# Kernel optimization log

Hardware: AMD Instinct MI355X
Metric: run time of the kernel (lower is better)

The kernel has to match this reference:

```python
import jax, jax.numpy as jnp
import numpy as np

DECAY = 0.99
EPS = 1e-05


def setup_inputs() -> dict:
    key = jax.random.key(0)
    k1, k2 = jax.random.split(key)
    B, L, D, K = 8, 2048, 512, 4096
    x = jax.random.normal(k1, (B, L, D), dtype=jnp.float32)
    # variance_scaling(scale=1, fan_in, uniform): U(-limit, limit), limit = sqrt(3/fan_in)
    limit = np.sqrt(3.0 / D)
    codebook = jax.random.uniform(k2, (K, D), dtype=jnp.float32, minval=-limit, maxval=limit)
    return {
        "x": x,
        "codebook": codebook,
        "hidden_cluster": jnp.zeros((K,), jnp.float32),
        "hidden_dw": jnp.zeros((K, D), jnp.float32),
        "count": jnp.zeros((), jnp.float32),
    }


def reference(x, codebook, hidden_cluster, hidden_dw, count):
    K, D = codebook.shape
    B, L, _ = x.shape
    # avoids materializing the (B,L,K,D) broadcast the naive cdist creates)
    x2 = jnp.sum(x * x, axis=-1, keepdims=True)                  # (B,L,1)
    c2 = jnp.sum(codebook * codebook, axis=-1)                   # (K,)
    xc = jnp.einsum("bld,kd->blk", x, codebook)                  # (B,L,K)
    d2 = x2 - 2.0 * xc + c2
    indices = jnp.argmin(d2, axis=-1)                            # (B,L) int
    flat_idx = indices.reshape(-1)

    # cluster_counts = one_hot(indices).sum((0,1)) as a scatter-add
    cluster_counts = jnp.zeros((K,), jnp.float32).at[flat_idx].add(1.0)
    # dw = einsum('bln,bld->nd', one_hot, x) as a scatter-add of x rows
    dw = jnp.zeros((K, D), jnp.float32).at[flat_idx].add(x.reshape(-1, D))

    decay = jnp.asarray(DECAY, x.dtype)
    one = jnp.ones([], x.dtype)
    count_new = count + 1.0
    bias = one - decay ** count_new

    hidden_cluster_new = hidden_cluster * decay + (one - decay) * cluster_counts
    avg_cluster = hidden_cluster_new / bias
    hidden_dw_new = hidden_dw * decay + (one - decay) * dw
    avg_dw = hidden_dw_new / bias

    N = jnp.sum(avg_cluster)
    cc = (avg_cluster + EPS) / (N + K * EPS) * N
    codebook_new = avg_dw / cc[:, None]

    # quantized = one_hot(indices) @ codebook_new == gather
    q = codebook_new[indices]                                    # (B,L,D)
    quantized = x + jax.lax.stop_gradient(q - x)
    # optax.l2_loss(x, quantized).mean() == 0.5*(x-quantized)^2 mean
    codebook_loss = 0.5 * jnp.mean(jnp.square(x - quantized))
    return quantized, codebook_loss, indices
```

## Files before the change

kernel.cpp:

```cpp
#include <hip/hip_runtime.h>
#include <math.h>

#define BL 16384
#define D  512
#define K  4096
#define NCHB 8
#define XLOFF 8388608

#define OFF_C2    0
#define OFF_X2    (16<<10)
#define OFF_CNT   (80<<10)
#define OFF_AVGC  (96<<10)
#define OFF_SCAL  (112<<10)
#define OFF_IDX16 (116<<10)
#define OFF_KEYS  (160<<10)
#define OFF_CAND  (288<<10)
#define OFF_CBP   (576<<10)
#define OFF_CBN_FB (256<<10)

typedef _Float16 f16x8 __attribute__((ext_vector_type(8)));
typedef float    f32x4 __attribute__((ext_vector_type(4)));
#define MFMA16(a,b,c) __builtin_amdgcn_mfma_f32_16x16x32_f16(a,b,c,0,0,0)


__global__ void rowsq_all(const float* __restrict__ x, const float* __restrict__ cb,
                          float* __restrict__ x2, float* __restrict__ c2)
{
    int b    = blockIdx.x;
    int lane = threadIdx.x;
    const float* p; float* o; int row;
    if (b < K) { p = cb; o = c2; row = b; }
    else       { p = x;  o = x2; row = b - K; }
    p += (size_t)row * D;
    float s = 0.f;
#pragma unroll
    for (int j = 0; j < D / 64; ++j) {
        float v = p[lane + j * 64];
        s = fmaf(v, v, s);
    }
#pragma unroll
    for (int off = 32; off > 0; off >>= 1)
        s += __shfl_down(s, off, 64);
    if (lane == 0) o[row] = s;
}

__global__ __launch_bounds__(256) void rescore_kernel(
    const float* __restrict__ x, const float* __restrict__ cb,
    const float* __restrict__ x2, const float* __restrict__ c2,
    const unsigned short* __restrict__ cand,
    unsigned long long* __restrict__ keys,
    float* __restrict__ counts, unsigned short* __restrict__ idx16)
{
    int t = blockIdx.x * 256 + threadIdx.x;
    int row = t >> 3, ci = t & 7;
    int idx = cand[(size_t)row * 8 + ci];
    const float* xp = x  + (size_t)row * D;
    const float* cp = cb + (size_t)idx * D;
    float acc = 0.f;
#pragma unroll 4
    for (int k0 = 0; k0 < D; k0 += 4) {
        float4 xv = *(const float4*)(xp + k0);
        float4 cv = *(const float4*)(cp + k0);
        acc = fmaf(xv.x, cv.x, acc);
        acc = fmaf(xv.y, cv.y, acc);
        acc = fmaf(xv.z, cv.z, acc);
        acc = fmaf(xv.w, cv.w, acc);
    }
    float wv = x2[row] - 2.0f * acc;
    float dd = wv + c2[idx];
    unsigned long long key =
        ((unsigned long long)__float_as_uint(dd) << 12) | (unsigned long long)idx;
#pragma unroll
    for (int m = 1; m < 8; m <<= 1) {
        unsigned long long o = __shfl_xor(key, m, 64);
        key = o < key ? o : key;
    }
    if ((t & 7) == 0) {
        keys[row] = key;
        int kf = (int)(key & 0xFFFULL);
        idx16[row] = (unsigned short)kf;
        atomicAdd(&counts[kf], 1.0f);
    }
}


__device__ __forceinline__ void load_lds16(const unsigned short* g, unsigned short* l) {
    __builtin_amdgcn_global_load_lds(
        (const __attribute__((address_space(1))) unsigned int*)(g),
        (__attribute__((address_space(3))) unsigned int*)(l), 16, 0, 0);
}

__global__ __launch_bounds__(256) void split_interleave(
    const float* __restrict__ x, const float* __restrict__ cb,
    unsigned short* __restrict__ xp, unsigned short* __restrict__ cbp)
{
    int gw   = blockIdx.x * 4 + (threadIdx.x >> 6);
    int lane = threadIdx.x & 63;
    int rl   = lane >> 3;
    int p    = lane & 7;
    const float* src; int nr, c, r0; bool isX;
    if (gw < 16384) { c = gw >> 11; r0 = (gw & 2047) * 8; src = x;  nr = BL; isX = true; }
    else { int lw = gw - 16384; c = lw >> 9; r0 = (lw & 511) * 8; src = cb; nr = K; isX = false; }
    int r = r0 + rl;
    int g = p ^ rl;
    const float* sp = src + (size_t)r * D + c * 64 + g * 8;
    float4 f0 = *(const float4*)sp, f1 = *(const float4*)(sp + 4);
    float f[8] = {f0.x,f0.y,f0.z,f0.w,f1.x,f1.y,f1.z,f1.w};
    __align__(16) _Float16 oh[8], ol[8];
#pragma unroll
    for (int i = 0; i < 8; ++i) {
        _Float16 h = (_Float16)f[i];
        oh[i] = h;
        ol[i] = (_Float16)(f[i] - (float)h);
    }
    size_t off = ((size_t)(c * nr + r) * 8 + p) * 8;
    if (isX) {
        *(uint4*)(xp + off)         = *(const uint4*)oh;
        *(uint4*)(xp + XLOFF + off) = *(const uint4*)ol;
    } else {
        *(uint4*)(cbp + off) = *(const uint4*)oh;
    }
}

__global__ __launch_bounds__(512, 2) void argmin_mfma(
    const unsigned short* __restrict__ xp, const unsigned short* __restrict__ cbp,
    const float* __restrict__ x2, const float* __restrict__ c2,
    unsigned short* __restrict__ cand)
{
    __shared__ __align__(16) unsigned short buf[2 * 32768];
    __shared__ __align__(16) float c2s[1024];
    __shared__ __align__(16) float x2s[128];

#define AH_OFF 0
#define AL_OFF 16384
#define B_OFF  32768

    const int tid = threadIdx.x;
    const int l   = tid & 63;
    const int q   = l >> 4;
    const int cc  = l & 15;
    const int w   = tid >> 6;
    const int wm  = w >> 2;
    const int wn  = w & 3;
    const int row0 = blockIdx.x * 128;
    const int nb   = blockIdx.y * 1024;

    char* sb = (char*)buf;

    int rdA[4], rdB[4];
#pragma unroll
    for (int t = 0; t < 4; ++t) {
        int ra = wm * 64 + t * 16 + cc;
        int rb = wn * 64 + t * 16 + cc;
        rdA[t] = ra * 128 + ((q ^ (ra & 7)) * 16);
        rdB[t] = rb * 128 + ((q ^ (rb & 7)) * 16);
    }

    if (tid < 128) x2s[tid] = x2[row0 + tid];
#pragma unroll
    for (int j = 0; j < 2; ++j) c2s[tid + j * 512] = c2[nb + tid + j * 512];
    {
        const unsigned short* sAh0 = xp + ((size_t)row0 << 6);
        const unsigned short* sAl0 = sAh0 + XLOFF;
        const unsigned short* sB0  = cbp + ((size_t)nb << 6);
#pragma unroll
        for (int i = 0; i < 2; ++i) {
            load_lds16(sAh0 + i * 4096 + tid * 8,
                       (unsigned short*)(sb + AH_OFF + i * 8192 + tid * 16));
            load_lds16(sAl0 + i * 4096 + tid * 8,
                       (unsigned short*)(sb + AL_OFF + i * 8192 + tid * 16));
        }
#pragma unroll
        for (int i = 0; i < 4; ++i)
            load_lds16(sB0 + i * 4096 + tid * 8,
                       (unsigned short*)(sb + B_OFF + i * 8192 + tid * 16));
    }
    asm volatile("s_waitcnt vmcnt(0) lgkmcnt(0)" ::: "memory");
    __builtin_amdgcn_s_barrier();

    unsigned long long k1[16], k2[16];
#pragma unroll
    for (int s = 0; s < 16; ++s) { k1[s] = ~0ULL; k2[s] = ~0ULL; }

    f32x4 acc[4][4];
#pragma unroll
    for (int tm = 0; tm < 4; ++tm)
#pragma unroll
        for (int tn = 0; tn < 4; ++tn) { f32x4 z = {0.f,0.f,0.f,0.f}; acc[tm][tn] = z; }

#pragma unroll 1
    for (int it = 0; it < 32; ++it) {
        const bool pf = (it < 31);
        const int  br = (it & 1) << 16;
        const int  bw = br ^ 65536;
        const int  it1 = it + 1;
        const int  c1  = it1 & 7;
        const int  n01 = (it1 >> 3) & 3;
        const unsigned short* srcAh = xp + ((size_t)(c1 * BL + row0) << 6);
        const unsigned short* srcAl = srcAh + XLOFF;
        const unsigned short* srcB  = cbp + ((size_t)(c1 * K + nb + n01 * 256) << 6);

        f16x8 Ah[4], Bf[4];
#pragma unroll
        for (int t = 0; t < 4; ++t) {
            Ah[t] = *(const f16x8*)(sb + br + AH_OFF + rdA[t]);
            Bf[t] = *(const f16x8*)(sb + br + B_OFF  + rdB[t]);
        }
        if (pf) {
#pragma unroll
            for (int i = 0; i < 2; ++i)
                load_lds16(srcAh + i * 4096 + tid * 8,
                           (unsigned short*)(sb + bw + AH_OFF + i * 8192 + tid * 16));
            asm volatile("s_waitcnt vmcnt(2)" ::: "memory");
        } else {
            asm volatile("s_waitcnt vmcnt(0)" ::: "memory");
        }
        __builtin_amdgcn_s_barrier();
        asm volatile("s_waitcnt lgkmcnt(0)" ::: "memory");
        __builtin_amdgcn_sched_barrier(0);
        __builtin_amdgcn_s_setprio(1);
#pragma unroll
        for (int tm = 0; tm < 4; ++tm)
#pragma unroll
            for (int tn = 0; tn < 4; ++tn)
                acc[tm][tn] = MFMA16(Ah[tm], Bf[tn], acc[tm][tn]);
        __builtin_amdgcn_s_setprio(0);
        __builtin_amdgcn_s_barrier();

        f16x8 Al[4];
#pragma unroll
        for (int t = 0; t < 4; ++t)
            Al[t] = *(const f16x8*)(sb + br + AL_OFF + rdA[t]);
        if (pf) {
#pragma unroll
            for (int i = 0; i < 2; ++i)
                load_lds16(srcB + i * 4096 + tid * 8,
                           (unsigned short*)(sb + bw + B_OFF + i * 8192 + tid * 16));
        }
        __builtin_amdgcn_s_barrier();
        asm volatile("s_waitcnt lgkmcnt(0)" ::: "memory");
        __builtin_amdgcn_sched_barrier(0);
        __builtin_amdgcn_s_setprio(1);
#pragma unroll
        for (int tm = 0; tm < 4; ++tm)
#pragma unroll
            for (int tn = 0; tn < 4; ++tn)
                acc[tm][tn] = MFMA16(Al[tm], Bf[tn], acc[tm][tn]);
        __builtin_amdgcn_s_setprio(0);
        __builtin_amdgcn_s_barrier();

        f16x8 Ah1[4], Bg[4];
#pragma unroll
        for (int t = 0; t < 4; ++t) {
            Ah1[t] = *(const f16x8*)(sb + br + AH_OFF + (rdA[t] ^ 64));
            Bg[t]  = *(const f16x8*)(sb + br + B_OFF  + (rdB[t] ^ 64));
        }
        if (pf) {
#pragma unroll
            for (int i = 2; i < 4; ++i)
                load_lds16(srcB + i * 4096 + tid * 8,
                           (unsigned short*)(sb + bw + B_OFF + i * 8192 + tid * 16));
        }
        __builtin_amdgcn_s_barrier();
        asm volatile("s_waitcnt lgkmcnt(0)" ::: "memory");
        __builtin_amdgcn_sched_barrier(0);
        __builtin_amdgcn_s_setprio(1);
#pragma unroll
        for (int tm = 0; tm < 4; ++tm)
#pragma unroll
            for (int tn = 0; tn < 4; ++tn)
                acc[tm][tn] = MFMA16(Ah1[tm], Bg[tn], acc[tm][tn]);
        __builtin_amdgcn_s_setprio(0);
        __builtin_amdgcn_s_barrier();

        f16x8 Al1[4];
#pragma unroll
        for (int t = 0; t < 4; ++t)
            Al1[t] = *(const f16x8*)(sb + br + AL_OFF + (rdA[t] ^ 64));
        if (pf) {
#pragma unroll
            for (int i = 0; i < 2; ++i)
                load_lds16(srcAl + i * 4096 + tid * 8,
                           (unsigned short*)(sb + bw + AL_OFF + i * 8192 + tid * 16));
            asm volatile("s_waitcnt vmcnt(2)" ::: "memory");
        }
        __builtin_amdgcn_s_barrier();
        asm volatile("s_waitcnt lgkmcnt(0)" ::: "memory");
        __builtin_amdgcn_sched_barrier(0);
        __builtin_amdgcn_s_setprio(1);
#pragma unroll
        for (int tm = 0; tm < 4; ++tm)
#pragma unroll
            for (int tn = 0; tn < 4; ++tn)
                acc[tm][tn] = MFMA16(Al1[tm], Bg[tn], acc[tm][tn]);
        __builtin_amdgcn_s_setprio(0);
        __builtin_amdgcn_s_barrier();

        if ((it & 7) == 7) {
            const int n0 = it >> 3;
            float c2v[4];
#pragma unroll
            for (int tn = 0; tn < 4; ++tn)
                c2v[tn] = c2s[n0 * 256 + wn * 64 + tn * 16 + cc];
#pragma unroll
            for (int tm = 0; tm < 4; ++tm)
#pragma unroll
                for (int r = 0; r < 4; ++r) {
                    const int s = tm * 4 + r;
                    float x2v = x2s[wm * 64 + tm * 16 + q * 4 + r];
#pragma unroll
                    for (int tn = 0; tn < 4; ++tn) {
                        unsigned col = nb + n0 * 256 + wn * 64 + tn * 16 + cc;
                        float dd = (x2v - 2.0f * acc[tm][tn][r]) + c2v[tn];
                        unsigned long long key =
                            ((unsigned long long)__float_as_uint(dd) << 12) | col;
                        if (key < k1[s]) { k2[s] = k1[s]; k1[s] = key; }
                        else if (key < k2[s]) { k2[s] = key; }
                    }
                }
#pragma unroll
            for (int tm = 0; tm < 4; ++tm)
#pragma unroll
                for (int tn = 0; tn < 4; ++tn) { f32x4 z = {0.f,0.f,0.f,0.f}; acc[tm][tn] = z; }
        }
    }

#pragma unroll
    for (int s = 0; s < 16; ++s) {
#pragma unroll
        for (int m = 1; m < 16; m <<= 1) {
            unsigned long long o1 = __shfl_xor(k1[s], m, 64);
            unsigned long long o2 = __shfl_xor(k2[s], m, 64);
            unsigned long long lf = k1[s] > o1 ? k1[s] : o1;
            unsigned long long ws_ = k2[s] < o2 ? k2[s] : o2;
            k1[s] = k1[s] < o1 ? k1[s] : o1;
            k2[s] = lf < ws_ ? lf : ws_;
        }
    }

    __syncthreads();
    unsigned long long* sc = (unsigned long long*)buf;
    if (cc == 0) {
#pragma unroll
        for (int s = 0; s < 16; ++s) {
            int rl = wm * 64 + (s >> 2) * 16 + q * 4 + (s & 3);
            sc[(rl * 4 + wn) * 2 + 0] = k1[s];
            sc[(rl * 4 + wn) * 2 + 1] = k2[s];
        }
    }
    __syncthreads();
    if (tid < 128) {
        unsigned long long m1 = sc[(tid * 4 + 0) * 2 + 0];
        unsigned long long m2 = sc[(tid * 4 + 0) * 2 + 1];
#pragma unroll
        for (int j = 1; j < 4; ++j) {
            unsigned long long b1 = sc[(tid * 4 + j) * 2 + 0];
            unsigned long long b2 = sc[(tid * 4 + j) * 2 + 1];
            unsigned long long lf = m1 > b1 ? m1 : b1;
            unsigned long long ws_ = m2 < b2 ? m2 : b2;
            m1 = m1 < b1 ? m1 : b1;
            m2 = lf < ws_ ? lf : ws_;
        }
        size_t base = (size_t)(row0 + tid) * 8 + blockIdx.y * 2;
        cand[base + 0] = (unsigned short)(m1 & 0xFFFULL);
        cand[base + 1] = (unsigned short)(m2 & 0xFFFULL);
    }
}

__global__ __launch_bounds__(256) void argmin_fb(
    const float* __restrict__ x, const float* __restrict__ cb,
    const float* __restrict__ x2, const float* __restrict__ c2,
    unsigned long long* __restrict__ keys)
{
    __shared__ __align__(16) float As[32][68];
    __shared__ __align__(16) float Bs[32][68];
    __shared__ float rv[64][16];
    __shared__ int   ri[64][16];

    const int tid  = threadIdx.x;
    const int tx   = tid & 15;
    const int ty   = tid >> 4;
    const int row0 = blockIdx.x * 64;
    const int nb   = blockIdx.y * 1024;

    float x2r[4];
#pragma unroll
    for (int m = 0; m < 4; ++m) x2r[m] = x2[row0 + ty * 4 + m];

    float minv[4]; int mini[4];
#pragma unroll
    for (int m = 0; m < 4; ++m) { minv[m] = 3.4028235e38f; mini[m] = 0; }

    for (int n0 = 0; n0 < 1024; n0 += 64) {
        float acc[4][4];
#pragma unroll
        for (int m = 0; m < 4; ++m)
#pragma unroll
            for (int n = 0; n < 4; ++n) acc[m][n] = 0.f;

        for (int d0 = 0; d0 < D; d0 += 32) {
            __syncthreads();
#pragma unroll
            for (int j = 0; j < 2; ++j) {
                int v   = j * 256 + tid;
                int row = v >> 3;
                int col = (v & 7) * 4;
                float4 av = *(const float4*)(x  + (size_t)(row0 + row) * D + d0 + col);
                As[col + 0][row] = av.x; As[col + 1][row] = av.y;
                As[col + 2][row] = av.z; As[col + 3][row] = av.w;
                float4 bv = *(const float4*)(cb + (size_t)(nb + n0 + row) * D + d0 + col);
                Bs[col + 0][row] = bv.x; Bs[col + 1][row] = bv.y;
                Bs[col + 2][row] = bv.z; Bs[col + 3][row] = bv.w;
            }
            __syncthreads();
#pragma unroll
            for (int kk = 0; kk < 32; ++kk) {
                float4 a4 = *(const float4*)&As[kk][ty * 4];
                float4 b4 = *(const float4*)&Bs[kk][tx * 4];
                float a_[4] = { a4.x, a4.y, a4.z, a4.w };
                float b_[4] = { b4.x, b4.y, b4.z, b4.w };
#pragma unroll
                for (int m = 0; m < 4; ++m)
#pragma unroll
                    for (int n = 0; n < 4; ++n)
                        acc[m][n] = fmaf(a_[m], b_[n], acc[m][n]);
            }
        }
#pragma unroll
        for (int n = 0; n < 4; ++n) {
            int kidx = nb + n0 + tx * 4 + n;
            float c2k = c2[kidx];
#pragma unroll
            for (int m = 0; m < 4; ++m) {
                float wv = x2r[m] - 2.0f * acc[m][n];
                float dd = wv + c2k;
                if (dd < minv[m]) { minv[m] = dd; mini[m] = kidx; }
            }
        }
    }
#pragma unroll
    for (int m = 0; m < 4; ++m) { rv[ty * 4 + m][tx] = minv[m]; ri[ty * 4 + m][tx] = mini[m]; }
    __syncthreads();
    if (tid < 64) {
        float bv = rv[tid][0]; int bi = ri[tid][0];
#pragma unroll
        for (int j = 1; j < 16; ++j) {
            float v = rv[tid][j]; int ii = ri[tid][j];
            if (v < bv || (v == bv && ii < bi)) { bv = v; bi = ii; }
        }
        unsigned long long key =
            ((unsigned long long)__float_as_uint(bv) << 12) | (unsigned long long)bi;
        atomicMin(&keys[row0 + tid], key);
    }
}


__global__ void count_kernel(const unsigned long long* __restrict__ keys,
                             float* __restrict__ counts, unsigned short* __restrict__ idx16)
{
    int i = blockIdx.x * 256 + threadIdx.x;
    int k = (int)(keys[i] & 0xFFFULL);
    idx16[i] = (unsigned short)k;
    atomicAdd(&counts[k], 1.0f);
}

__global__ __launch_bounds__(256) void ema_cluster_kernel(
    const float* __restrict__ hc, const float* __restrict__ counts,
    const float* __restrict__ countp, float* __restrict__ avgc, float* __restrict__ Nout)
{
    __shared__ float sm[256];
    int i = blockIdx.x * 256 + threadIdx.x;
    const float om = 1.0f - 0.99f;
    float bias = 1.0f - powf(0.99f, countp[0] + 1.0f);
    float a = (hc[i] * 0.99f + om * counts[i]) / bias;
    avgc[i] = a;
    sm[threadIdx.x] = a;
    __syncthreads();
    for (int s = 128; s > 0; s >>= 1) {
        if (threadIdx.x < s) sm[threadIdx.x] += sm[threadIdx.x + s];
        __syncthreads();
    }
    if (threadIdx.x == 0) atomicAdd(Nout, sm[0]);
}

__global__ __launch_bounds__(256) void code_update_kernel(
    const float* __restrict__ x, const unsigned short* __restrict__ idx16,
    const float* __restrict__ hdw, const float* __restrict__ avgc,
    const float* __restrict__ Nptr, const float* __restrict__ countp,
    float* __restrict__ cbn)
{
    __shared__ unsigned short rows[2048];
    __shared__ int cnt;
    int k = blockIdx.x, tid = threadIdx.x;
    if (tid == 0) cnt = 0;
    __syncthreads();
    const uint4* ip = (const uint4*)idx16;
    for (int j = 0; j < 8; ++j) {
        int u = j * 256 + tid;
        uint4 v = ip[u];
        unsigned ww[4] = {v.x, v.y, v.z, v.w};
#pragma unroll
        for (int e = 0; e < 4; ++e) {
            int k0 = (int)(ww[e] & 0xFFFFu), k1 = (int)(ww[e] >> 16);
            if (k0 == k) { int p = atomicAdd(&cnt, 1); if (p < 2048) rows[p] = (unsigned short)(u * 8 + e * 2); }
            if (k1 == k) { int p = atomicAdd(&cnt, 1); if (p < 2048) rows[p] = (unsigned short)(u * 8 + e * 2 + 1); }
        }
    }
    __syncthreads();
    int n = cnt < 2048 ? cnt : 2048;
    float a0 = 0.f, a1 = 0.f;
    for (int p = 0; p < n; ++p) {
        int r = rows[p];
        a0 += x[(size_t)r * D + tid];
        a1 += x[(size_t)r * D + tid + 256];
    }
    const float om = 1.0f - 0.99f;
    float bias = 1.0f - powf(0.99f, countp[0] + 1.0f);
    float Nv = *Nptr;
    float ccv = ((avgc[k] + 1e-5f) / (Nv + 0.04096f)) * Nv;
    size_t b = (size_t)k * D;
    cbn[b + tid]       = ((hdw[b + tid]       * 0.99f + om * a0) / bias) / ccv;
    cbn[b + tid + 256] = ((hdw[b + tid + 256] * 0.99f + om * a1) / bias) / ccv;
}

__global__ __launch_bounds__(256) void gather_kernel(
    const float* __restrict__ x, const unsigned long long* __restrict__ keys,
    const float* __restrict__ cbn, float* __restrict__ outq,
    float* __restrict__ partial)
{
    __shared__ float sm[256];
    int row = blockIdx.x;
    int tid = threadIdx.x;
    int k   = (int)(keys[row] & 0xFFFULL);
    const float* xpp = x   + (size_t)row * D;
    const float* cp  = cbn + (size_t)k   * D;
    float* op = outq + (size_t)row * D;
    float local = 0.f;
#pragma unroll
    for (int j = 0; j < 2; ++j) {
        int d = tid + j * 256;
        float xv = xpp[d];
        float qv = cp[d];
        float quant = xv + (qv - xv);
        op[d] = quant;
        float diff = xv - quant;
        local = fmaf(diff, diff, local);
    }
    sm[tid] = local;
    __syncthreads();
    for (int s = 128; s > 0; s >>= 1) {
        if (tid < s) sm[tid] += sm[tid + s];
        __syncthreads();
    }
    if (tid == 0) {
        partial[row] = sm[0];
        outq[8388609 + row] = (float)k;
    }
}

__global__ __launch_bounds__(256) void finalize_kernel(
    const float* __restrict__ partial, float* __restrict__ out)
{
    __shared__ double sm[256];
    int tid = threadIdx.x;
    double s = 0.0;
#pragma unroll
    for (int j = 0; j < 64; ++j) s += (double)partial[tid + j * 256];
    sm[tid] = s;
    __syncthreads();
    for (int st = 128; st > 0; st >>= 1) {
        if (tid < st) sm[tid] += sm[tid + st];
        __syncthreads();
    }
    if (tid == 0) out[8388608] = (float)(0.5 * sm[0] / 8388608.0);
}


extern "C" void kernel_launch(void* const* d_in, const int* in_sizes, int n_in,
                              void* d_out, int out_size, void* d_ws, size_t ws_size,
                              hipStream_t stream)
{
    const float* x   = (const float*)d_in[0];
    const float* cb  = (const float*)d_in[1];
    const float* hc  = (const float*)d_in[2];
    const float* hdw = (const float*)d_in[3];
    const float* cnt = (const float*)d_in[4];
    float* out = (float*)d_out;

    char* ws = (char*)d_ws;
    float*  c2     = (float*)(ws + OFF_C2);
    float*  x2     = (float*)(ws + OFF_X2);
    float*  counts = (float*)(ws + OFF_CNT);
    float*  avgc   = (float*)(ws + OFF_AVGC);
    float*  Nout   = (float*)(ws + OFF_SCAL + 8);
    unsigned short* idx16 = (unsigned short*)(ws + OFF_IDX16);
    unsigned long long* keys = (unsigned long long*)(ws + OFF_KEYS);
    float*  partial= (float*)(ws + OFF_X2);

    hipMemsetAsync(ws + OFF_CNT, 0, (32 << 10) + 16, stream);

    rowsq_all<<<K + BL, 64, 0, stream>>>(x, cb, x2, c2);

    const bool primary = ws_size >= ((size_t)10 << 20);
    float* cbn;
    if (primary) {
        unsigned short* gxp = (unsigned short*)d_out;
        unsigned short* gcp = (unsigned short*)(ws + OFF_CBP);
        unsigned short* cand = (unsigned short*)(ws + OFF_CAND);
        cbn = (float*)(ws + OFF_CBP);

        split_interleave<<<5120, 256, 0, stream>>>(x, cb, gxp, gcp);
        argmin_mfma<<<dim3(BL / 128, 4), 512, 0, stream>>>(gxp, gcp, x2, c2, cand);
        rescore_kernel<<<(BL * 8) / 256, 256, 0, stream>>>(x, cb, x2, c2, cand, keys,
                                                           counts, idx16);
    } else {
        cbn = (float*)(ws + OFF_CBN_FB);
        hipMemsetAsync(ws + OFF_KEYS, 0xFF, BL * 8, stream);
        argmin_fb<<<dim3(BL / 64, 4), 256, 0, stream>>>(x, cb, x2, c2, keys);
        count_kernel<<<BL / 256, 256, 0, stream>>>(keys, counts, idx16);
    }

    ema_cluster_kernel<<<K / 256, 256, 0, stream>>>(hc, counts, cnt, avgc, Nout);
    code_update_kernel<<<K, 256, 0, stream>>>(x, idx16, hdw, avgc, Nout, cnt, cbn);
    gather_kernel<<<BL, 256, 0, stream>>>(x, keys, cbn, out, partial);
    finalize_kernel<<<1, 256, 0, stream>>>(partial, out);
}
```

Before: 349.5 us.

## Issue all next-stage LDS prefetches upfront and use one barrier per iteration

```diff
diff --git a/kernel.cpp b/kernel.cpp
--- a/kernel.cpp
+++ b/kernel.cpp
@@ -193,12 +193,28 @@
         const bool pf = (it < 31);
         const int  br = (it & 1) << 16;
         const int  bw = br ^ 65536;
-        const int  it1 = it + 1;
-        const int  c1  = it1 & 7;
-        const int  n01 = (it1 >> 3) & 3;
-        const unsigned short* srcAh = xp + ((size_t)(c1 * BL + row0) << 6);
-        const unsigned short* srcAl = srcAh + XLOFF;
-        const unsigned short* srcB  = cbp + ((size_t)(c1 * K + nb + n01 * 256) << 6);
+
+        if (pf) {
+            const int it1 = it + 1;
+            const int c1  = it1 & 7;
+            const int n01 = (it1 >> 3) & 3;
+            const unsigned short* srcAh = xp + ((size_t)(c1 * BL + row0) << 6);
+            const unsigned short* srcAl = srcAh + XLOFF;
+            const unsigned short* srcB  = cbp + ((size_t)(c1 * K + nb + n01 * 256) << 6);
+#pragma unroll
+            for (int i = 0; i < 2; ++i)
+                load_lds16(srcAh + i * 4096 + tid * 8,
+                           (unsigned short*)(sb + bw + AH_OFF + i * 8192 + tid * 16));
+#pragma unroll
+            for (int i = 0; i < 2; ++i)
+                load_lds16(srcAl + i * 4096 + tid * 8,
+                           (unsigned short*)(sb + bw + AL_OFF + i * 8192 + tid * 16));
+#pragma unroll
+            for (int i = 0; i < 4; ++i)
+                load_lds16(srcB + i * 4096 + tid * 8,
+                           (unsigned short*)(sb + bw + B_OFF + i * 8192 + tid * 16));
+            __builtin_amdgcn_sched_barrier(0);
+        }
 
         f16x8 Ah[4], Bf[4];
 #pragma unroll
@@ -206,48 +222,21 @@
             Ah[t] = *(const f16x8*)(sb + br + AH_OFF + rdA[t]);
             Bf[t] = *(const f16x8*)(sb + br + B_OFF  + rdB[t]);
         }
-        if (pf) {
-#pragma unroll
-            for (int i = 0; i < 2; ++i)
-                load_lds16(srcAh + i * 4096 + tid * 8,
-                           (unsigned short*)(sb + bw + AH_OFF + i * 8192 + tid * 16));
-            asm volatile("s_waitcnt vmcnt(2)" ::: "memory");
-        } else {
-            asm volatile("s_waitcnt vmcnt(0)" ::: "memory");
-        }
-        __builtin_amdgcn_s_barrier();
-        asm volatile("s_waitcnt lgkmcnt(0)" ::: "memory");
-        __builtin_amdgcn_sched_barrier(0);
-        __builtin_amdgcn_s_setprio(1);
 #pragma unroll
         for (int tm = 0; tm < 4; ++tm)
 #pragma unroll
             for (int tn = 0; tn < 4; ++tn)
                 acc[tm][tn] = MFMA16(Ah[tm], Bf[tn], acc[tm][tn]);
-        __builtin_amdgcn_s_setprio(0);
-        __builtin_amdgcn_s_barrier();
 
         f16x8 Al[4];
 #pragma unroll
         for (int t = 0; t < 4; ++t)
             Al[t] = *(const f16x8*)(sb + br + AL_OFF + rdA[t]);
-        if (pf) {
-#pragma unroll
-            for (int i = 0; i < 2; ++i)
-                load_lds16(srcB + i * 4096 + tid * 8,
-                           (unsigned short*)(sb + bw + B_OFF + i * 8192 + tid * 16));
-        }
-        __builtin_amdgcn_s_barrier();
-        asm volatile("s_waitcnt lgkmcnt(0)" ::: "memory");
-        __builtin_amdgcn_sched_barrier(0);
-        __builtin_amdgcn_s_setprio(1);
 #pragma unroll
         for (int tm = 0; tm < 4; ++tm)
 #pragma unroll
             for (int tn = 0; tn < 4; ++tn)
                 acc[tm][tn] = MFMA16(Al[tm], Bf[tn], acc[tm][tn]);
-        __builtin_amdgcn_s_setprio(0);
-        __builtin_amdgcn_s_barrier();
 
         f16x8 Ah1[4], Bg[4];
 #pragma unroll
@@ -255,46 +244,21 @@
             Ah1[t] = *(const f16x8*)(sb + br + AH_OFF + (rdA[t] ^ 64));
             Bg[t]  = *(const f16x8*)(sb + br + B_OFF  + (rdB[t] ^ 64));
         }
-        if (pf) {
-#pragma unroll
-            for (int i = 2; i < 4; ++i)
-                load_lds16(srcB + i * 4096 + tid * 8,
-                           (unsigned short*)(sb + bw + B_OFF + i * 8192 + tid * 16));
-        }
-        __builtin_amdgcn_s_barrier();
-        asm volatile("s_waitcnt lgkmcnt(0)" ::: "memory");
-        __builtin_amdgcn_sched_barrier(0);
-        __builtin_amdgcn_s_setprio(1);
 #pragma unroll
         for (int tm = 0; tm < 4; ++tm)
 #pragma unroll
             for (int tn = 0; tn < 4; ++tn)
                 acc[tm][tn] = MFMA16(Ah1[tm], Bg[tn], acc[tm][tn]);
-        __builtin_amdgcn_s_setprio(0);
-        __builtin_amdgcn_s_barrier();
 
         f16x8 Al1[4];
 #pragma unroll
         for (int t = 0; t < 4; ++t)
             Al1[t] = *(const f16x8*)(sb + br + AL_OFF + (rdA[t] ^ 64));
-        if (pf) {
-#pragma unroll
-            for (int i = 0; i < 2; ++i)
-                load_lds16(srcAl + i * 4096 + tid * 8,
-                           (unsigned short*)(sb + bw + AL_OFF + i * 8192 + tid * 16));
-            asm volatile("s_waitcnt vmcnt(2)" ::: "memory");
-        }
-        __builtin_amdgcn_s_barrier();
-        asm volatile("s_waitcnt lgkmcnt(0)" ::: "memory");
-        __builtin_amdgcn_sched_barrier(0);
-        __builtin_amdgcn_s_setprio(1);
 #pragma unroll
         for (int tm = 0; tm < 4; ++tm)
 #pragma unroll
             for (int tn = 0; tn < 4; ++tn)
                 acc[tm][tn] = MFMA16(Al1[tm], Bg[tn], acc[tm][tn]);
-        __builtin_amdgcn_s_setprio(0);
-        __builtin_amdgcn_s_barrier();
 
         if ((it & 7) == 7) {
             const int n0 = it >> 3;
@@ -323,6 +287,9 @@
 #pragma unroll
                 for (int tn = 0; tn < 4; ++tn) { f32x4 z = {0.f,0.f,0.f,0.f}; acc[tm][tn] = z; }
         }
+
+        asm volatile("s_waitcnt vmcnt(0)" ::: "memory");
+        __builtin_amdgcn_s_barrier();
     }
 
 #pragma unroll
```

After: 355.8 us. No clear change (+1.8%).
